# Performance work log

Measured on AMD Instinct MI355X. Metric: run time of the kernel, lower is better.

The kernel has to match this reference:

```python
import jax, jax.numpy as jnp
import numpy as np

N, K, P, A, NBINS, RP = 4096, 48, 128, 5, 16, 32
LN_EPS = 1e-5

def _normalize(v, eps=1e-6):
    return v / jnp.sqrt(jnp.maximum((v * v).sum(-1, keepdims=True), eps))

def extract_frames(pos):
    # pos: [N, A, 3]; atom order N, CA, C, ... -> Gram-Schmidt backbone frame
    n, ca, c = pos[:, 0], pos[:, 1], pos[:, 2]
    e1 = _normalize(c - ca)
    v2 = n - ca
    e2 = _normalize(v2 - (v2 * e1).sum(-1, keepdims=True) * e1)
    e3 = jnp.cross(e1, e2)
    R = jnp.stack([e1, e2, e3], axis=-1)  # [N,3,3], columns = frame axes
    return R, ca

def distance_rbf(d, d_min=0.0, d_max=22.0, bins=NBINS):
    step = (d_max - d_min) / bins
    centers = d_min + step * jnp.arange(bins, dtype=d.dtype)
    return jnp.exp(-(((d[..., None] - centers) / step) ** 2))

def relpos_features(resi, chain, batch, neighbours):
    # clipped relative sequence position, extra class for cross-chain/batch pairs
    rel = jnp.clip(resi[neighbours] - resi[:, None], -RP, RP) + RP
    same = (chain[neighbours] == chain[:, None]) & (batch[neighbours] == batch[:, None])
    cls = jnp.where(same, rel, 2 * RP + 1)
    return jax.nn.one_hot(cls, 2 * RP + 2, dtype=jnp.float32)  # [N,K,66]

def distance_features(pos, neighbours):
    pn = pos[neighbours]  # [N,K,A,3] gather
    diff = pos[:, None, :, None] - pn[:, :, None, :]  # [N,K,A,A,3]
    d = jnp.sqrt(jnp.maximum((diff * diff).sum(-1), 1e-12))
    return distance_rbf(d).reshape(N, K, A * A * NBINS)

def direction_features(pos, neighbours, R, ca):
    rel = pos[neighbours] - ca[:, None, None]  # [N,K,A,3]
    local = jnp.einsum('nji,nkaj->nkai', R, rel)  # express in frame of residue i
    return _normalize(local).reshape(N, K, A * 3)

def rotation_features(neighbours, R):
    Rrel = jnp.einsum('nji,nkjl->nkil', R, R[neighbours])  # R_i^T R_j
    return Rrel.reshape(N, K, 9)

def pair_vector_features(pos, neighbours, R, ca):
    rel = pos[neighbours] - ca[:, None, None]
    local = jnp.einsum('nji,nkaj->nkai', R, rel)
    return local.reshape(N, K, A * 3)

def setup_inputs() -> dict:
    key = jax.random.key(0)
    ks = jax.random.split(key, 12)
    s = 0.02
    pos = 5.0 * jax.random.normal(ks[0], (N, A, 3), dtype=jnp.float32)
    dmap = 22.0 * jax.random.uniform(ks[1], (N, N), dtype=jnp.float32)
    mask = jnp.ones((N,), dtype=jnp.float32)
    neighbours = jax.random.randint(ks[2], (N, K), 0, N, dtype=jnp.int32)
    resi = jnp.arange(N, dtype=jnp.int32)
    chain = jnp.zeros((N,), dtype=jnp.int32)
    batch = jnp.zeros((N,), dtype=jnp.int32)
    W_relpos = s * jax.random.normal(ks[3], (2 * RP + 2, P), dtype=jnp.float32)
    W_dmap = s * jax.random.normal(ks[4], (NBINS, P), dtype=jnp.float32)
    W_dist = s * jax.random.normal(ks[5], (A * A * NBINS, P), dtype=jnp.float32)
    W_dir = s * jax.random.normal(ks[6], (3 * A, P), dtype=jnp.float32)
    W_rot = s * jax.random.normal(ks[7], (9, P), dtype=jnp.float32)
    W_vec = s * jax.random.normal(ks[8], (3 * A, P), dtype=jnp.float32)
    ln_scale = jnp.ones((P,), dtype=jnp.float32)
    ln_offset = jnp.zeros((P,), dtype=jnp.float32)
    W1 = s * jax.random.normal(ks[9], (P, 2 * P), dtype=jnp.float32)
    b1 = jnp.zeros((2 * P,), dtype=jnp.float32)
    W2 = s * jax.random.normal(ks[10], (2 * P, P), dtype=jnp.float32)
    b2 = jnp.zeros((P,), dtype=jnp.float32)
    return dict(pos=pos, dmap=dmap, mask=mask, W_relpos=W_relpos, W_dmap=W_dmap,
                W_dist=W_dist, W_dir=W_dir, W_rot=W_rot, W_vec=W_vec,
                ln_scale=ln_scale, ln_offset=ln_offset, W1=W1, b1=b1, W2=W2, b2=b2,
                neighbours=neighbours, resi=resi, chain=chain, batch=batch)

def reference(pos, dmap, mask, W_relpos, W_dmap, W_dist, W_dir, W_rot, W_vec,
              ln_scale, ln_offset, W1, b1, W2, b2, neighbours, resi, chain, batch):
    pair_mask = mask[:, None] * mask[neighbours] * (neighbours != -1).astype(mask.dtype)
    R, ca = extract_frames(pos)
    idx = jnp.arange(N)
    dmap_nb = dmap[idx[:, None], neighbours]  # [N,K] gather of distance map
    # multi-branch linear sum
    pair = relpos_features(resi, chain, batch, neighbours) @ W_relpos
    pair += jnp.where(pair_mask[..., None] > 0, distance_rbf(dmap_nb), 0.0) @ W_dmap
    pair += distance_features(pos, neighbours) @ W_dist
    pair += direction_features(pos, neighbours, R, ca) @ W_dir
    pair += rotation_features(neighbours, R) @ W_rot
    pair += pair_vector_features(pos, neighbours, R, ca) @ W_vec
    # LayerNorm (create_scale=True, create_offset=True)
    mu = pair.mean(-1, keepdims=True)
    var = ((pair - mu) ** 2).mean(-1, keepdims=True)
    pair = (pair - mu) / jnp.sqrt(var + LN_EPS) * ln_scale + ln_offset
    # MLP(2P -> P) with gelu
    pair = jax.nn.gelu(pair @ W1 + b1) @ W2 + b2
    return pair, pair_mask
```

## Files before the change

kernel.cpp:

```cpp
#include <hip/hip_runtime.h>
#include <hip/hip_bf16.h>

#define N_RES 4096
#define KNB   48
#define PCH   128
#define INV_STEP 0.727272727272727f
#define E2INV 0.13533528323661270f

typedef __bf16 bf16x8 __attribute__((ext_vector_type(8)));
typedef float  f32x4  __attribute__((ext_vector_type(4)));

#define FOCT(o,m) (((o)*49 + (m))*8)

__device__ __align__(16) unsigned short g_wcat[60*128*8];
__device__ __align__(16) unsigned short g_w1[16*256*8];
__device__ __align__(16) unsigned short g_w2[32*128*8];

__device__ __forceinline__ unsigned short f2bf(float f) {
  unsigned int u = __float_as_uint(f);
  return (unsigned short)((u + 0x7fffu + ((u >> 16) & 1u)) >> 16);
}
__device__ __forceinline__ unsigned int pk2(float a, float b) {
  __hip_bfloat162 h = __float22bfloat162_rn(make_float2(a, b));
  unsigned int u; __builtin_memcpy(&u, &h, 4); return u;
}
__device__ __forceinline__ float gelu_f(float x) {
  float p = x * x;
  float q = fmaf(p, 0.044715f, 1.0f);
  float r = x * q;
  float e = __expf(-1.5957691216057308f * r);
  return x * __builtin_amdgcn_rcpf(1.0f + e);
}
__device__ __forceinline__ void frame_from_pos(const float* p, float* R) {
  float cax = p[3], cay = p[4], caz = p[5];
  float e1x = p[6]-cax, e1y = p[7]-cay, e1z = p[8]-caz;
  float i1 = __builtin_amdgcn_rsqf(fmaxf(e1x*e1x + e1y*e1y + e1z*e1z, 1e-6f));
  e1x *= i1; e1y *= i1; e1z *= i1;
  float vx = p[0]-cax, vy = p[1]-cay, vz = p[2]-caz;
  float dp = vx*e1x + vy*e1y + vz*e1z;
  float e2x = vx - dp*e1x, e2y = vy - dp*e1y, e2z = vz - dp*e1z;
  float i2 = __builtin_amdgcn_rsqf(fmaxf(e2x*e2x + e2y*e2y + e2z*e2z, 1e-6f));
  e2x *= i2; e2y *= i2; e2z *= i2;
  float e3x = e1y*e2z - e1z*e2y;
  float e3y = e1z*e2x - e1x*e2z;
  float e3z = e1x*e2y - e1y*e2x;
  R[0]=e1x; R[1]=e2x; R[2]=e3x;
  R[3]=e1y; R[4]=e2y; R[5]=e3y;
  R[6]=e1z; R[7]=e2z; R[8]=e3z;
}

__device__ __forceinline__ void stage_bins(unsigned short* sF, const float* s_xall,
                                           int xbase, int ntasks, int t) {
  for (int i = t; i < ntasks; i += 256) {
    int rloc = i / 48;
    int m = i - 48*rloc;
    float x = fminf(s_xall[(xbase + rloc)*48 + m], 25.0f);
    float u  = __expf(-x*x);
    float wu = __expf(2.0f*x - 1.0f);
    float xm = x - 15.0f;
    float d  = __expf(-xm*xm);
    float wd = __expf(-2.0f*xm - 1.0f);
    float bins[16];
    bins[0] = u;
    #pragma unroll
    for (int b = 1; b < 16; ++b) { u *= wu; wu *= E2INV; bins[b] = u; }
    bins[15] = fmaxf(bins[15], d);
    #pragma unroll
    for (int b = 14; b >= 0; --b) { d *= wd; wd *= E2INV; bins[b] = fmaxf(bins[b], d); }
    unsigned int p0 = pk2(bins[0], bins[1]),  p1 = pk2(bins[2], bins[3]);
    unsigned int p2 = pk2(bins[4], bins[5]),  p3 = pk2(bins[6], bins[7]);
    unsigned int p4 = pk2(bins[8], bins[9]),  p5 = pk2(bins[10], bins[11]);
    unsigned int p6 = pk2(bins[12], bins[13]),p7 = pk2(bins[14], bins[15]);
    int base = FOCT(2*rloc, m);
    *(uint4*)(sF + base)       = make_uint4(p0,p1,p2,p3);
    *(uint4*)(sF + base + 392) = make_uint4(p4,p5,p6,p7);
  }
}

__global__ __launch_bounds__(256) void prep_weights(
    const float* __restrict__ W_dmap, const float* __restrict__ W_dist,
    const float* __restrict__ W_dir, const float* __restrict__ W_rot,
    const float* __restrict__ W_vec, const float* __restrict__ W1,
    const float* __restrict__ W2)
{
  int i = blockIdx.x*256 + threadIdx.x;
  unsigned short pk[8];
  if (i < 7680) {
    int oct = i >> 7, col = i & 127;
    #pragma unroll
    for (int j = 0; j < 8; ++j) {
      int k = oct*8 + j;
      float v;
      if      (k < 16)  v = W_dmap[k*128 + col];
      else if (k < 416) v = W_dist[(k-16)*128 + col];
      else if (k < 431) v = W_dir[(k-416)*128 + col];
      else if (k < 446) v = W_vec[(k-431)*128 + col];
      else if (k < 455) v = W_rot[(k-446)*128 + col];
      else              v = 0.0f;
      pk[j] = f2bf(v);
    }
    *(uint4*)(g_wcat + i*8) = *(uint4*)pk;
  } else if (i < 11776) {
    int j2 = i - 7680;
    int oct = j2 >> 8, col = j2 & 255;
    #pragma unroll
    for (int j = 0; j < 8; ++j) {
      int k = oct*8 + j;
      int h = 32*(k>>5) + (k&1)*16 + ((k&31)>>1);
      pk[j] = f2bf(W1[h*256 + col]);
    }
    *(uint4*)(g_w1 + j2*8) = *(uint4*)pk;
  } else if (i < 15872) {
    int j3 = i - 11776;
    int oct = j3 >> 7, col = j3 & 127;
    #pragma unroll
    for (int j = 0; j < 8; ++j) {
      int k = oct*8 + j;
      int kh = k & 127;
      int h = (k>>7)*128 + 32*(kh>>5) + (kh&1)*16 + ((kh&31)>>1);
      pk[j] = f2bf(W2[h*128 + col]);
    }
    *(uint4*)(g_w2 + j3*8) = *(uint4*)pk;
  }
}

#define MFMA6(A0,A1,A2,B0,B1,ACC) \
  ACC[0][0] = __builtin_amdgcn_mfma_f32_16x16x32_bf16(A0, B0, ACC[0][0], 0,0,0); \
  ACC[1][0] = __builtin_amdgcn_mfma_f32_16x16x32_bf16(A1, B0, ACC[1][0], 0,0,0); \
  ACC[2][0] = __builtin_amdgcn_mfma_f32_16x16x32_bf16(A2, B0, ACC[2][0], 0,0,0); \
  ACC[0][1] = __builtin_amdgcn_mfma_f32_16x16x32_bf16(A0, B1, ACC[0][1], 0,0,0); \
  ACC[1][1] = __builtin_amdgcn_mfma_f32_16x16x32_bf16(A1, B1, ACC[1][1], 0,0,0); \
  ACC[2][1] = __builtin_amdgcn_mfma_f32_16x16x32_bf16(A2, B1, ACC[2][1], 0,0,0);

__global__ __launch_bounds__(256, 6) void fused_struct_kernel(
    const float* __restrict__ pos, const float* __restrict__ dmap,
    const float* __restrict__ mask, const float* __restrict__ W_relpos,
    const float* __restrict__ ln_scale, const float* __restrict__ ln_offset,
    const float* __restrict__ b1, const float* __restrict__ b2,
    const int* __restrict__ neighbours, const int* __restrict__ resi,
    const int* __restrict__ chain, const int* __restrict__ batch,
    float* __restrict__ out)
{
  const int n = blockIdx.x;
  const int t = threadIdx.x;
  const int lane = t & 63;
  const int wv   = t >> 6;
  const int ln15 = lane & 15;
  const int quad = lane >> 4;

  __shared__ __align__(16) char regF[12544];
  __shared__ __align__(16) char regP[12544];
  __shared__ __align__(16) float2 s_stats[48];

  unsigned short* sF    = (unsigned short*)regF;
  unsigned short* sPair = (unsigned short*)regP;
  float*  s_posnb = (float*)regP;
  float*  s_Rnb   = (float*)(regP + 3072);
  float*  s_xall  = (float*)(regP + 5376);
  float*  s_posn  = (float*)(regP + 10368);
  float*  s_Rn    = (float*)(regP + 10432);
  int*    s_cls   = (int*)  (regP + 10496);
  float2* s_part  = (float2*)(regP + 10752);

  if (t < KNB) {
    const int k = t;
    const int nbraw = neighbours[n*KNB + k];
    int nb = nbraw; if (nb < 0) nb += N_RES;
    float p[15];
    const float* pp = pos + nb*15;
    #pragma unroll
    for (int d = 0; d < 15; ++d) { p[d] = pp[d]; s_posnb[k*16+d] = p[d]; }
    float R[9];
    frame_from_pos(p, R);
    #pragma unroll
    for (int d = 0; d < 9; ++d) s_Rnb[k*12+d] = R[d];

    float pm = mask[n] * mask[nb] * ((nbraw != -1) ? 1.0f : 0.0f);
    out[N_RES*KNB*PCH + n*KNB + k] = pm;

    int rel = resi[nb] - resi[n];
    rel = (rel < -32) ? -32 : (rel > 32 ? 32 : rel);
    rel += 32;
    bool same = (chain[nb] == chain[n]) && (batch[nb] == batch[n]);
    s_cls[k] = same ? rel : 65;

    float xd = dmap[(long long)n*N_RES + nb] * INV_STEP;
    s_xall[k] = (pm > 0.0f) ? xd : 30.0f;
  } else if (t == 255) {
    float p[15];
    const float* pp = pos + n*15;
    #pragma unroll
    for (int d = 0; d < 15; ++d) { p[d] = pp[d]; s_posn[d] = p[d]; }
    float R[9];
    frame_from_pos(p, R);
    #pragma unroll
    for (int d = 0; d < 9; ++d) s_Rn[d] = R[d];
  }
  __syncthreads();

  for (int idx = t; idx < 1200; idx += 256) {
    int c = idx / 48, k = idx - 48*c;
    int a1 = c / 5, a2 = c - 5*a1;
    float dx = s_posn[a1*3+0] - s_posnb[k*16 + a2*3+0];
    float dy = s_posn[a1*3+1] - s_posnb[k*16 + a2*3+1];
    float dz = s_posn[a1*3+2] - s_posnb[k*16 + a2*3+2];
    float d2 = dx*dx + dy*dy + dz*dz;
    s_xall[48 + idx] = sqrtf(fmaxf(d2, 1e-12f)) * INV_STEP;
  }
  __syncthreads();

  f32x4 acc1[3][2] = {};

  #pragma unroll 1
  for (int st = 0; st < 3; ++st) {
    stage_bins(sF, s_xall, st*8, 384, t);
    __syncthreads();
    #pragma unroll
    for (int kc = 0; kc < 4; ++kc) {
      const unsigned short* ab = sF + FOCT(kc*4 + quad, ln15);
      bf16x8 a0 = *(const bf16x8*)(ab);
      bf16x8 a1 = *(const bf16x8*)(ab + 128);
      bf16x8 a2 = *(const bf16x8*)(ab + 256);
      const unsigned short* bb = g_wcat + (((st*4+kc)*4 + quad)*128 + 32*wv + ln15)*8;
      bf16x8 b0 = *(const bf16x8*)(bb);
      bf16x8 b1v= *(const bf16x8*)(bb + 128);
      MFMA6(a0,a1,a2,b0,b1v,acc1)
    }
    __syncthreads();
  }

  for (int i = t; i < 147; i += 256) ((uint4*)sF)[441 + i] = make_uint4(0,0,0,0);
  stage_bins(sF, s_xall, 24, 96, t);
  for (int idx = t; idx < 240; idx += 256) {
    int k = idx / 5, a = idx - 5*k;
    float rx = s_posnb[k*16 + a*3+0] - s_posn[3];
    float ry = s_posnb[k*16 + a*3+1] - s_posn[4];
    float rz = s_posnb[k*16 + a*3+2] - s_posn[5];
    float l0 = s_Rn[0]*rx + s_Rn[3]*ry + s_Rn[6]*rz;
    float l1 = s_Rn[1]*rx + s_Rn[4]*ry + s_Rn[7]*rz;
    float l2 = s_Rn[2]*rx + s_Rn[5]*ry + s_Rn[8]*rz;
    float inv = __builtin_amdgcn_rsqf(fmaxf(l0*l0 + l1*l1 + l2*l2, 1e-6f));
    int lv = 47 + a*3, ld = 32 + a*3;
    sF[FOCT(lv>>3,k) + (lv&7)] = f2bf(l0);
    lv++; sF[FOCT(lv>>3,k) + (lv&7)] = f2bf(l1);
    lv++; sF[FOCT(lv>>3,k) + (lv&7)] = f2bf(l2);
    sF[FOCT(ld>>3,k) + (ld&7)] = f2bf(l0*inv);
    ld++; sF[FOCT(ld>>3,k) + (ld&7)] = f2bf(l1*inv);
    ld++; sF[FOCT(ld>>3,k) + (ld&7)] = f2bf(l2*inv);
  }
  for (int idx = t; idx < 480; idx += 256) {
    int k = idx / 10, il = idx - 10*k;
    float v = 0.0f;
    if (il < 9) {
      int i2 = il / 3, l2c = il - 3*i2;
      v = s_Rn[0+i2]*s_Rnb[k*12 + 0+l2c]
        + s_Rn[3+i2]*s_Rnb[k*12 + 3+l2c]
        + s_Rn[6+i2]*s_Rnb[k*12 + 6+l2c];
    }
    int l = 62 + il;
    sF[FOCT(l>>3,k) + (l&7)] = f2bf(v);
  }
  __syncthreads();
  #pragma unroll
  for (int kc = 0; kc < 3; ++kc) {
    const unsigned short* ab = sF + FOCT(kc*4 + quad, ln15);
    bf16x8 a0 = *(const bf16x8*)(ab);
    bf16x8 a1 = *(const bf16x8*)(ab + 128);
    bf16x8 a2 = *(const bf16x8*)(ab + 256);
    const unsigned short* bb = g_wcat + (((12+kc)*4 + quad)*128 + 32*wv + ln15)*8;
    bf16x8 b0 = *(const bf16x8*)(bb);
    bf16x8 b1v= *(const bf16x8*)(bb + 128);
    MFMA6(a0,a1,a2,b0,b1v,acc1)
  }

  {
    int c0 = 32*wv + ln15;
    #pragma unroll
    for (int mt = 0; mt < 3; ++mt)
      #pragma unroll
      for (int r = 0; r < 4; ++r) {
        int row = mt*16 + quad*4 + r;
        const float* wr = W_relpos + s_cls[row]*128 + c0;
        acc1[mt][0][r] += wr[0];
        acc1[mt][1][r] += wr[16];
      }
  }

  #pragma unroll
  for (int mt = 0; mt < 3; ++mt)
    #pragma unroll
    for (int r = 0; r < 4; ++r) {
      float a0v = acc1[mt][0][r], a1v = acc1[mt][1][r];
      float sv = a0v + a1v;
      float qv = a0v*a0v + a1v*a1v;
      #pragma unroll
      for (int msk = 1; msk < 16; msk <<= 1) {
        sv += __shfl_xor(sv, msk);
        qv += __shfl_xor(qv, msk);
      }
      if (ln15 == 0) s_part[wv*48 + mt*16 + quad*4 + r] = make_float2(sv, qv);
    }
  __syncthreads();
  if (t < 48) {
    float S = 0.0f, Q = 0.0f;
    #pragma unroll
    for (int w = 0; w < 4; ++w) { float2 p = s_part[w*48 + t]; S += p.x; Q += p.y; }
    float mu = S * (1.0f/128.0f);
    float var = Q * (1.0f/128.0f) - mu*mu;
    s_stats[t] = make_float2(mu, __builtin_amdgcn_rsqf(var + 1e-5f));
  }
  __syncthreads();
  {
    int c0 = 32*wv + ln15;
    float gg0 = ln_scale[c0],  gg1 = ln_scale[c0+16];
    float oo0 = ln_offset[c0], oo1 = ln_offset[c0+16];
    int kp = 32*wv + 2*ln15;
    int oct = kp >> 3, slot = kp & 7;
    #pragma unroll
    for (int mt = 0; mt < 3; ++mt)
      #pragma unroll
      for (int r = 0; r < 4; ++r) {
        int row = mt*16 + quad*4 + r;
        float2 stt = s_stats[row];
        float v0 = (acc1[mt][0][r] - stt.x)*stt.y*gg0 + oo0;
        float v1 = (acc1[mt][1][r] - stt.x)*stt.y*gg1 + oo1;
        *(unsigned int*)(sPair + FOCT(oct,row) + slot) = pk2(v0, v1);
      }
  }
  __syncthreads();

  f32x4 acc3[3][2] = {};
  #pragma unroll 1
  for (int half = 0; half < 2; ++half) {
    f32x4 acc2[3][2] = {};
    #pragma unroll
    for (int kc = 0; kc < 4; ++kc) {
      const unsigned short* ab = sPair + FOCT(kc*4 + quad, ln15);
      bf16x8 a0 = *(const bf16x8*)(ab);
      bf16x8 a1 = *(const bf16x8*)(ab + 128);
      bf16x8 a2 = *(const bf16x8*)(ab + 256);
      const unsigned short* bb = g_w1 + ((kc*4 + quad)*256 + half*128 + 32*wv + ln15)*8;
      bf16x8 b0 = *(const bf16x8*)(bb);
      bf16x8 b1v= *(const bf16x8*)(bb + 128);
      MFMA6(a0,a1,a2,b0,b1v,acc2)
    }
    __syncthreads();
    {
      int hc = half*128 + 32*wv + ln15;
      float bb0 = b1[hc], bb1 = b1[hc+16];
      int kp = 32*wv + 2*ln15;
      int oct = kp >> 3, slot = kp & 7;
      #pragma unroll
      for (int mt = 0; mt < 3; ++mt)
        #pragma unroll
        for (int r = 0; r < 4; ++r) {
          int row = mt*16 + quad*4 + r;
          float h0 = gelu_f(acc2[mt][0][r] + bb0);
          float h1 = gelu_f(acc2[mt][1][r] + bb1);
          *(unsigned int*)(sF + FOCT(oct,row) + slot) = pk2(h0, h1);
        }
    }
    __syncthreads();
    #pragma unroll
    for (int kc = 0; kc < 4; ++kc) {
      const unsigned short* ab = sF + FOCT(kc*4 + quad, ln15);
      bf16x8 a0 = *(const bf16x8*)(ab);
      bf16x8 a1 = *(const bf16x8*)(ab + 128);
      bf16x8 a2 = *(const bf16x8*)(ab + 256);
      const unsigned short* bb = g_w2 + (((half*4 + kc)*4 + quad)*128 + 32*wv + ln15)*8;
      bf16x8 b0 = *(const bf16x8*)(bb);
      bf16x8 b1v= *(const bf16x8*)(bb + 128);
      MFMA6(a0,a1,a2,b0,b1v,acc3)
    }
  }

  {
    int c0 = 32*wv + ln15;
    float bo0 = b2[c0], bo1 = b2[c0+16];
    #pragma unroll
    for (int mt = 0; mt < 3; ++mt)
      #pragma unroll
      for (int r = 0; r < 4; ++r) {
        int row = mt*16 + quad*4 + r;
        out[(n*KNB + row)*PCH + c0]      = acc3[mt][0][r] + bo0;
        out[(n*KNB + row)*PCH + c0 + 16] = acc3[mt][1][r] + bo1;
      }
  }
}

extern "C" void kernel_launch(void* const* d_in, const int* in_sizes, int n_in,
                              void* d_out, int out_size, void* d_ws, size_t ws_size,
                              hipStream_t stream) {
  const float* pos       = (const float*)d_in[0];
  const float* dmap      = (const float*)d_in[1];
  const float* mask      = (const float*)d_in[2];
  const float* W_relpos  = (const float*)d_in[3];
  const float* W_dmap    = (const float*)d_in[4];
  const float* W_dist    = (const float*)d_in[5];
  const float* W_dir     = (const float*)d_in[6];
  const float* W_rot     = (const float*)d_in[7];
  const float* W_vec     = (const float*)d_in[8];
  const float* ln_scale  = (const float*)d_in[9];
  const float* ln_offset = (const float*)d_in[10];
  const float* W1        = (const float*)d_in[11];
  const float* b1        = (const float*)d_in[12];
  const float* W2        = (const float*)d_in[13];
  const float* b2        = (const float*)d_in[14];
  const int* neighbours  = (const int*)d_in[15];
  const int* resi        = (const int*)d_in[16];
  const int* chain       = (const int*)d_in[17];
  const int* batch       = (const int*)d_in[18];
  float* out = (float*)d_out;

  hipLaunchKernelGGL(prep_weights, dim3(62), dim3(256), 0, stream,
                     W_dmap, W_dist, W_dir, W_rot, W_vec, W1, W2);
  hipLaunchKernelGGL(fused_struct_kernel, dim3(N_RES), dim3(256), 0, stream,
                     pos, dmap, mask, W_relpos, ln_scale, ln_offset, b1, b2,
                     neighbours, resi, chain, batch, out);
}
```

Before: 276.4 us.

## Repack geometric features into aligned octets, pad smem strides, prefetch relpos rows

Reorders the concatenated weight rows so each atom's direction and pair-vector features fill one 8-wide octet, with rotation features in their own octets. The feature-staging threads can then write whole 16-byte packed bf16 vectors instead of many scalar bf16 stores, and the separate zero-fill pass is dropped. Shared-memory strides for the neighbour positions and frames are padded (16→17, 12→13) to reduce bank conflicts. The W_relpos gathers are issued early into registers so their global latency overlaps the MFMA stages, at the cost of 24 extra live registers per thread.

```diff
diff --git a/kernel.cpp b/kernel.cpp
--- a/kernel.cpp
+++ b/kernel.cpp
@@ -93,9 +93,12 @@
       float v;
       if      (k < 16)  v = W_dmap[k*128 + col];
       else if (k < 416) v = W_dist[(k-16)*128 + col];
-      else if (k < 431) v = W_dir[(k-416)*128 + col];
-      else if (k < 446) v = W_vec[(k-431)*128 + col];
-      else if (k < 455) v = W_rot[(k-446)*128 + col];
+      else if (k < 456) {
+        int a = (k-416) >> 3, jj = (k-416) & 7;
+        v = (jj < 3) ? W_dir[(a*3+jj)*128 + col]
+          : (jj < 6) ? W_vec[(a*3+jj-3)*128 + col] : 0.0f;
+      }
+      else if (k < 465) v = W_rot[(k-456)*128 + col];
       else              v = 0.0f;
       pk[j] = f2bf(v);
     }
@@ -155,12 +158,12 @@
   unsigned short* sF    = (unsigned short*)regF;
   unsigned short* sPair = (unsigned short*)regP;
   float*  s_posnb = (float*)regP;
-  float*  s_Rnb   = (float*)(regP + 3072);
-  float*  s_xall  = (float*)(regP + 5376);
-  float*  s_posn  = (float*)(regP + 10368);
-  float*  s_Rn    = (float*)(regP + 10432);
-  int*    s_cls   = (int*)  (regP + 10496);
-  float2* s_part  = (float2*)(regP + 10752);
+  float*  s_Rnb   = (float*)(regP + 3264);
+  float*  s_xall  = (float*)(regP + 5760);
+  float*  s_posn  = (float*)(regP + 10752);
+  float*  s_Rn    = (float*)(regP + 10816);
+  int*    s_cls   = (int*)  (regP + 10880);
+  float2* s_part  = (float2*)(regP + 11072);
 
   if (t < KNB) {
     const int k = t;
@@ -169,11 +172,11 @@
     float p[15];
     const float* pp = pos + nb*15;
     #pragma unroll
-    for (int d = 0; d < 15; ++d) { p[d] = pp[d]; s_posnb[k*16+d] = p[d]; }
+    for (int d = 0; d < 15; ++d) { p[d] = pp[d]; s_posnb[k*17+d] = p[d]; }
     float R[9];
     frame_from_pos(p, R);
     #pragma unroll
-    for (int d = 0; d < 9; ++d) s_Rnb[k*12+d] = R[d];
+    for (int d = 0; d < 9; ++d) s_Rnb[k*13+d] = R[d];
 
     float pm = mask[n] * mask[nb] * ((nbraw != -1) ? 1.0f : 0.0f);
     out[N_RES*KNB*PCH + n*KNB + k] = pm;
@@ -201,11 +204,25 @@
   for (int idx = t; idx < 1200; idx += 256) {
     int c = idx / 48, k = idx - 48*c;
     int a1 = c / 5, a2 = c - 5*a1;
-    float dx = s_posn[a1*3+0] - s_posnb[k*16 + a2*3+0];
-    float dy = s_posn[a1*3+1] - s_posnb[k*16 + a2*3+1];
-    float dz = s_posn[a1*3+2] - s_posnb[k*16 + a2*3+2];
+    float dx = s_posn[a1*3+0] - s_posnb[k*17 + a2*3+0];
+    float dy = s_posn[a1*3+1] - s_posnb[k*17 + a2*3+1];
+    float dz = s_posn[a1*3+2] - s_posnb[k*17 + a2*3+2];
     float d2 = dx*dx + dy*dy + dz*dz;
     s_xall[48 + idx] = sqrtf(fmaxf(d2, 1e-12f)) * INV_STEP;
+  }
+
+  float rp0[12], rp1[12];
+  {
+    int c0 = 32*wv + ln15;
+    #pragma unroll
+    for (int mt = 0; mt < 3; ++mt)
+      #pragma unroll
+      for (int r = 0; r < 4; ++r) {
+        int row = mt*16 + quad*4 + r;
+        const float* wr = W_relpos + s_cls[row]*128 + c0;
+        rp0[mt*4+r] = wr[0];
+        rp1[mt*4+r] = wr[16];
+      }
   }
   __syncthreads();
 
@@ -229,36 +246,33 @@
     __syncthreads();
   }
 
-  for (int i = t; i < 147; i += 256) ((uint4*)sF)[441 + i] = make_uint4(0,0,0,0);
   stage_bins(sF, s_xall, 24, 96, t);
-  for (int idx = t; idx < 240; idx += 256) {
-    int k = idx / 5, a = idx - 5*k;
-    float rx = s_posnb[k*16 + a*3+0] - s_posn[3];
-    float ry = s_posnb[k*16 + a*3+1] - s_posn[4];
-    float rz = s_posnb[k*16 + a*3+2] - s_posn[5];
+  if (t < 240) {
+    int k = t / 5, a = t - 5*k;
+    float rx = s_posnb[k*17 + a*3+0] - s_posn[3];
+    float ry = s_posnb[k*17 + a*3+1] - s_posn[4];
+    float rz = s_posnb[k*17 + a*3+2] - s_posn[5];
     float l0 = s_Rn[0]*rx + s_Rn[3]*ry + s_Rn[6]*rz;
     float l1 = s_Rn[1]*rx + s_Rn[4]*ry + s_Rn[7]*rz;
     float l2 = s_Rn[2]*rx + s_Rn[5]*ry + s_Rn[8]*rz;
     float inv = __builtin_amdgcn_rsqf(fmaxf(l0*l0 + l1*l1 + l2*l2, 1e-6f));
-    int lv = 47 + a*3, ld = 32 + a*3;
-    sF[FOCT(lv>>3,k) + (lv&7)] = f2bf(l0);
-    lv++; sF[FOCT(lv>>3,k) + (lv&7)] = f2bf(l1);
-    lv++; sF[FOCT(lv>>3,k) + (lv&7)] = f2bf(l2);
-    sF[FOCT(ld>>3,k) + (ld&7)] = f2bf(l0*inv);
-    ld++; sF[FOCT(ld>>3,k) + (ld&7)] = f2bf(l1*inv);
-    ld++; sF[FOCT(ld>>3,k) + (ld&7)] = f2bf(l2*inv);
-  }
-  for (int idx = t; idx < 480; idx += 256) {
-    int k = idx / 10, il = idx - 10*k;
-    float v = 0.0f;
-    if (il < 9) {
+    *(uint4*)(sF + FOCT(4+a, k)) =
+        make_uint4(pk2(l0*inv, l1*inv), pk2(l2*inv, l0), pk2(l1, l2), 0u);
+  }
+  if (t >= 208) {
+    int k = t - 208;
+    float rr[9];
+    #pragma unroll
+    for (int il = 0; il < 9; ++il) {
       int i2 = il / 3, l2c = il - 3*i2;
-      v = s_Rn[0+i2]*s_Rnb[k*12 + 0+l2c]
-        + s_Rn[3+i2]*s_Rnb[k*12 + 3+l2c]
-        + s_Rn[6+i2]*s_Rnb[k*12 + 6+l2c];
-    }
-    int l = 62 + il;
-    sF[FOCT(l>>3,k) + (l&7)] = f2bf(v);
+      rr[il] = s_Rn[0+i2]*s_Rnb[k*13 + 0+l2c]
+             + s_Rn[3+i2]*s_Rnb[k*13 + 3+l2c]
+             + s_Rn[6+i2]*s_Rnb[k*13 + 6+l2c];
+    }
+    *(uint4*)(sF + FOCT(9, k))  = make_uint4(pk2(rr[0],rr[1]), pk2(rr[2],rr[3]),
+                                             pk2(rr[4],rr[5]), pk2(rr[6],rr[7]));
+    *(uint4*)(sF + FOCT(10, k)) = make_uint4(pk2(rr[8],0.0f), 0u, 0u, 0u);
+    *(uint4*)(sF + FOCT(11, k)) = make_uint4(0u, 0u, 0u, 0u);
   }
   __syncthreads();
   #pragma unroll
@@ -273,18 +287,13 @@
     MFMA6(a0,a1,a2,b0,b1v,acc1)
   }
 
-  {
-    int c0 = 32*wv + ln15;
-    #pragma unroll
-    for (int mt = 0; mt < 3; ++mt)
-      #pragma unroll
-      for (int r = 0; r < 4; ++r) {
-        int row = mt*16 + quad*4 + r;
-        const float* wr = W_relpos + s_cls[row]*128 + c0;
-        acc1[mt][0][r] += wr[0];
-        acc1[mt][1][r] += wr[16];
-      }
-  }
+  #pragma unroll
+  for (int mt = 0; mt < 3; ++mt)
+    #pragma unroll
+    for (int r = 0; r < 4; ++r) {
+      acc1[mt][0][r] += rp0[mt*4+r];
+      acc1[mt][1][r] += rp1[mt*4+r];
+    }
 
   #pragma unroll
   for (int mt = 0; mt < 3; ++mt)
```

New measurement: 293.7 us. +6.3%, slower.
